# Kernel tuning notes

Hardware: AMD Instinct MI355X
Metric: run time of the kernel (lower is better)

The kernel has to match this reference:

```python
import jax, jax.numpy as jnp
import numpy as np
from jax.scipy.special import gammaln

N, D, RDIM = 2048, 128, 16   # observations, obs dim, simplex dim
R_SAMP = 500                 # importance samples
SIGMA = 0.01
REG = 0.8


def dirichlet_logpdf(x, a):
    # x: [..., r] on simplex, a: broadcastable [..., r] concentrations
    return (jnp.sum((a - 1.0) * jnp.log(x), axis=-1)
            + gammaln(jnp.sum(a, axis=-1))
            - jnp.sum(gammaln(a), axis=-1))


def setup_inputs() -> dict:
    key = jax.random.key(0)
    k1, k2, k3, k4 = jax.random.split(key, 4)
    H = jax.random.uniform(k1, (D, RDIM), dtype=jnp.float32)          # endmember matrix, positive
    alpha = jax.random.uniform(k2, (RDIM,), dtype=jnp.float32) * 2.0 + 0.1
    # realistic observations: y = H z + noise with z ~ Dirichlet(alpha)
    z = jax.random.dirichlet(k3, alpha, shape=(N,)).astype(jnp.float32)  # [N, r]
    y = z @ H.T + jnp.sqrt(SIGMA) * jax.random.normal(k4, (N, D), dtype=jnp.float32)
    return {"y": y, "H": H, "alpha": alpha}


def reference(y, H, alpha):
    sigma = SIGMA
    alpha0 = alpha.sum()
    m = alpha / alpha0                                                  # [r]
    C = (jnp.diag(m) - jnp.outer(m, m)) / (alpha0 + 1.0)                # [r, r]
    EY = H @ m                                                          # [d]
    Cyy = H @ C @ H.T + sigma * jnp.eye(H.shape[0], dtype=jnp.float32)  # [d, d]
    invCyy = jnp.linalg.inv(Cyy)
    gain = C @ H.T @ invCyy                                             # [r, d]
    # LMMSE posterior mean per observation, projected back to simplex
    LMMSE_m = jax.nn.relu(m + (y - EY) @ gain.T) + 1e-6                 # [N, r]
    LMMSE_m = LMMSE_m / LMMSE_m.sum(axis=1, keepdims=True)
    LMMSE_C = C - gain @ H @ C                                          # [r, r]
    trace_C = jax.nn.relu(jnp.trace(LMMSE_C)) + 1e-6
    k = (1.0 - jnp.sum(LMMSE_m ** 2, axis=-1)) / trace_C - 1.0          # [N]
    diri = jax.nn.relu(k[:, None] * LMMSE_m) + REG                      # [N, r]
    # importance sampling: Dirichlet proposal (reparameterized in jax)
    samp = jax.random.dirichlet(jax.random.key(42), diri,
                                shape=(R_SAMP, y.shape[0])).astype(jnp.float32)  # [R, N, r]
    yzSy = jnp.einsum('dr,hnr->nhd', H, samp) - y[:, None, :]           # [N, R, d]
    pyz = jnp.sum(yzSy * yzSy, axis=-1) / (-2.0 * sigma)                # [N, R]
    qz = dirichlet_logpdf(samp, diri).T                                 # [N, R]
    pz = dirichlet_logpdf(samp, alpha).T                                # [N, R]
    weights = jax.nn.softmax(pyz + pz - qz, axis=-1)                    # [N, R]
    zy = jnp.einsum('hnk,nh->nk', samp, weights)                        # [N, r]
    zzy = jnp.einsum('hnk,hnl,nh->nkl', samp, samp, weights)            # [N, r, r]
    return zy, zzy
```

## Files before the change

kernel.cpp:

```cpp
#include <hip/hip_runtime.h>
#include <cstdint>
#include <cmath>

#pragma clang fp contract(off)

#define N_OBS 2048
#define D_DIM 128
#define R_DIM 16
#define NSAMP 500

#define WS_M     0
#define WS_EY    64
#define WS_GAIN  576
#define WS_SCAL  8768
#define WS_G     8800
#define WS_DIRI  279136
#define WS_QC    410208
#define WS_U     418400

__device__ __forceinline__ float flog(float x)   { return (float)log((double)x); }
__device__ __forceinline__ float flog1p(float x) { return (float)log1p((double)x); }

__device__ __forceinline__ void tf_block(uint32_t k0, uint32_t k1,
                                         uint32_t x0, uint32_t x1,
                                         uint32_t& o0, uint32_t& o1) {
  const uint32_t k2 = k0 ^ k1 ^ 0x1BD11BDAu;
  x0 += k0; x1 += k1;
#define TF_R(r) { x0 += x1; x1 = (x1 << (r)) | (x1 >> (32 - (r))); x1 ^= x0; }
  TF_R(13) TF_R(15) TF_R(26) TF_R(6)
  x0 += k1; x1 += k2 + 1u;
  TF_R(17) TF_R(29) TF_R(16) TF_R(24)
  x0 += k2; x1 += k0 + 2u;
  TF_R(13) TF_R(15) TF_R(26) TF_R(6)
  x0 += k0; x1 += k1 + 3u;
  TF_R(17) TF_R(29) TF_R(16) TF_R(24)
  x0 += k1; x1 += k2 + 4u;
  TF_R(13) TF_R(15) TF_R(26) TF_R(6)
  x0 += k2; x1 += k0 + 5u;
#undef TF_R
  o0 = x0; o1 = x1;
}

__device__ __forceinline__ uint32_t rb32(uint32_t ka, uint32_t kb) {
  uint32_t o0, o1;
  tf_block(ka, kb, 0u, 0u, o0, o1);
  return o0 ^ o1;
}

__device__ __forceinline__ float u01(uint32_t bits) {
  uint32_t fb = (bits >> 9) | 0x3F800000u;
  return __uint_as_float(fb) - 1.0f;
}

__device__ __forceinline__ float erfinv_xla(float x) {
  float w = -flog1p(-(x * x));
  float p;
  if (w < 5.0f) {
    w = w - 2.5f;
    p = 2.81022636e-08f;
    p = 3.43273939e-07f + p * w;
    p = -3.5233877e-06f + p * w;
    p = -4.39150654e-06f + p * w;
    p = 0.00021858087f + p * w;
    p = -0.00125372503f + p * w;
    p = -0.00417768164f + p * w;
    p = 0.246640727f + p * w;
    p = 1.50140941f + p * w;
  } else {
    w = sqrtf(w) - 3.0f;
    p = -0.000200214257f;
    p = 0.000100950558f + p * w;
    p = 0.00134934322f + p * w;
    p = -0.00367342844f + p * w;
    p = 0.00573950773f + p * w;
    p = -0.0076224613f + p * w;
    p = 0.00943887047f + p * w;
    p = 1.00167406f + p * w;
    p = 2.83297682f + p * w;
  }
  return p * x;
}

__device__ __forceinline__ float normal_jax(uint32_t ka, uint32_t kb) {
  float f = u01(rb32(ka, kb));
  float u = f * 2.0f + (-0.99999994f);
  u = fmaxf(-0.99999994f, u);
  return 1.41421356f * erfinv_xla(u);
}

__global__ __launch_bounds__(256) void prep_kernel(const float* __restrict__ H,
                                                   const float* __restrict__ alpha,
                                                   char* __restrict__ ws) {
  float* m    = (float*)(ws + WS_M);
  float* EY   = (float*)(ws + WS_EY);
  float* gain = (float*)(ws + WS_GAIN);
  float* scal = (float*)(ws + WS_SCAL);
  float* Gws  = (float*)(ws + WS_G);

  __shared__ float sH[128 * 16];
  __shared__ float sC[16][16];
  __shared__ float sHC[128 * 16];
  __shared__ float sm[16];
  __shared__ double sHtH[16][16];
  __shared__ double M[16][33];
  __shared__ double dfac[16];
  __shared__ double spiv;
  __shared__ int   spivrow;
  __shared__ float sgain[16 * 128];

  int t = threadIdx.x;
  for (int i = t; i < 2048; i += 256) sH[i] = H[i];
  __syncthreads();

  if (t == 0) {
    float a0 = 0.0f;
    for (int j = 0; j < 16; ++j) a0 += alpha[j];
    float pc = lgammaf(a0);
    for (int j = 0; j < 16; ++j) pc -= lgammaf(alpha[j]);
    scal[2] = a0; scal[1] = pc;
    for (int j = 0; j < 16; ++j) { sm[j] = alpha[j] / a0; m[j] = sm[j]; }
  }
  __syncthreads();
  float a0 = scal[2];

  {
    int i = t >> 4, j = t & 15;
    float v = ((i == j) ? sm[i] : 0.0f) - sm[i] * sm[j];
    sC[i][j] = v / (a0 + 1.0f);
  }
  if (t < 128) {
    float acc = 0.0f;
    for (int j = 0; j < 16; ++j) acc += sH[t * 16 + j] * sm[j];
    EY[t] = acc;
  }
  __syncthreads();

  for (int idx = t; idx < 2048; idx += 256) {
    int dd = idx >> 4, j = idx & 15;
    float acc = 0.0f;
    for (int i = 0; i < 16; ++i) acc += sH[dd * 16 + i] * sC[i][j];
    sHC[idx] = acc;
  }
  {
    int i = t >> 4, j = t & 15;
    double acc = 0.0;
    for (int dd = 0; dd < 128; ++dd)
      acc += (double)sH[dd * 16 + i] * (double)sH[dd * 16 + j];
    sHtH[i][j] = acc;
    Gws[i * 16 + j] = (float)acc;
  }
  __syncthreads();

  {
    int i = t >> 4, j = t & 15;
    double acc = (i == j) ? 0.01 : 0.0;
    for (int k = 0; k < 16; ++k) acc += (double)sC[i][k] * sHtH[k][j];
    M[i][j] = acc;
    M[i][16 + j] = (i == j) ? 1.0 : 0.0;
  }
  __syncthreads();

  for (int p = 0; p < 16; ++p) {
    if (t == 0) {
      int best = p; double bv = fabs(M[p][p]);
      for (int r = p + 1; r < 16; ++r) {
        double v = fabs(M[r][p]);
        if (v > bv) { bv = v; best = r; }
      }
      spivrow = best;
    }
    __syncthreads();
    int pr = spivrow;
    double va = 0.0, vb = 0.0;
    if (t < 32 && pr != p) { va = M[p][t]; vb = M[pr][t]; }
    __syncthreads();
    if (t < 32 && pr != p) { M[p][t] = vb; M[pr][t] = va; }
    __syncthreads();
    if (t == 0) spiv = 1.0 / M[p][p];
    __syncthreads();
    if (t < 32) M[p][t] *= spiv;
    if (t < 16) dfac[t] = M[t][p];
    __syncthreads();
    for (int e = t; e < 512; e += 256) {
      int r = e >> 5, c = e & 31;
      if (r != p) M[r][c] -= dfac[r] * M[p][c];
    }
    __syncthreads();
  }

  for (int idx = t; idx < 2048; idx += 256) {
    int j = idx >> 7, dd = idx & 127;
    double acc = 0.0;
    for (int k = 0; k < 16; ++k) acc += M[j][16 + k] * (double)sHC[dd * 16 + k];
    float g = (float)acc;
    sgain[j * 128 + dd] = g;
    gain[j * 128 + dd] = g;
  }
  __syncthreads();

  if (t == 0) {
    float tr = 0.0f;
    for (int j = 0; j < 16; ++j) {
      float s2 = 0.0f;
      for (int dd = 0; dd < 128; ++dd) s2 += sgain[j * 128 + dd] * sHC[dd * 16 + j];
      tr += sC[j][j] - s2;
    }
    tr = fmaxf(tr, 0.0f) + 1e-6f;
    scal[0] = tr;
  }
}

__global__ __launch_bounds__(256) void diri_kernel(const float* __restrict__ y,
                                                   const float* __restrict__ H,
                                                   char* __restrict__ ws) {
  float* m    = (float*)(ws + WS_M);
  float* EY   = (float*)(ws + WS_EY);
  float* gain = (float*)(ws + WS_GAIN);
  float* scal = (float*)(ws + WS_SCAL);
  float* diri = (float*)(ws + WS_DIRI);
  float* cns  = (float*)(ws + WS_QC);
  float* Uws  = (float*)(ws + WS_U);

  __shared__ float sg[16 * 128];
  __shared__ float sH[128 * 16];
  __shared__ float sEY[128];
  __shared__ float sm[16];
  __shared__ float s_tr, s_pc;

  int t = threadIdx.x;
  for (int i = t; i < 2048; i += 256) { sg[i] = gain[i]; sH[i] = H[i]; }
  if (t < 128) sEY[t] = EY[t];
  if (t < 16) sm[t] = m[t];
  if (t == 0) { s_tr = scal[0]; s_pc = scal[1]; }
  __syncthreads();

  int n = blockIdx.x * 256 + t;
  float tv[16], u[16];
#pragma unroll
  for (int j = 0; j < 16; ++j) { tv[j] = sm[j]; u[j] = 0.0f; }
  float yy = 0.0f;
  const float* yn = y + n * 128;
  for (int dd = 0; dd < 128; ++dd) {
    float yv = yn[dd];
    float dy = yv - sEY[dd];
    yy += yv * yv;
#pragma unroll
    for (int j = 0; j < 16; ++j) {
      tv[j] += dy * sg[j * 128 + dd];
      u[j]  += yv * sH[dd * 16 + j];
    }
  }
  float s = 0.0f;
#pragma unroll
  for (int j = 0; j < 16; ++j) { tv[j] = fmaxf(tv[j], 0.0f) + 1e-6f; s += tv[j]; }
  float ssq = 0.0f;
#pragma unroll
  for (int j = 0; j < 16; ++j) { tv[j] = tv[j] / s; ssq += tv[j] * tv[j]; }
  float k = (1.0f - ssq) / s_tr - 1.0f;
  float dsum = 0.0f, lgs = 0.0f;
  float* dn = diri + n * 16;
#pragma unroll
  for (int j = 0; j < 16; ++j) {
    float dj = fmaxf(k * tv[j], 0.0f) + 0.8f;
    dn[j] = dj; dsum += dj; lgs += lgammaf(dj);
    Uws[n * 16 + j] = u[j];
  }
  float qcn = lgammaf(dsum) - lgs;
  cns[n] = s_pc - qcn - 50.0f * yy;
}

__global__ __launch_bounds__(256) void main_kernel(const float* __restrict__ alpha,
                                                   const char* __restrict__ ws,
                                                   float* __restrict__ out) {
  const float* diri = (const float*)(ws + WS_DIRI);
  const float* cns  = (const float*)(ws + WS_QC);
  const float* Uw   = (const float*)(ws + WS_U);
  const float* Gw   = (const float*)(ws + WS_G);

  __shared__ float slg_all[32][256];
  __shared__ float sz[16][17];
  __shared__ float slw[16], swv[16];
  __shared__ float sM, sS, sFac;

  int t = threadIdx.x;
  int n = blockIdx.x;
  int h_sub = t >> 4, j = t & 15;

  float aj = diri[n * 16 + j];

  {
    bool boost = (aj >= 1.0f);
    float aa = boost ? aj : (aj + 1.0f);
    float d  = aa - 0.33333334f;
    float cc = 0.33333334f / sqrtf(d);
    float inv_a = 1.0f / aj;
    float ld32 = logf(d);
    int numc = (h_sub < 4) ? 32 : 31;
    int c = 0;
    bool need_init = true;
    bool pending = true;
    uint32_t kcx = 0, kcy = 0;
    float log_samples = 0.0f;

    while (__ballot(pending)) {
      if (pending) {
        if (need_init) {
          int h = c * 16 + h_sub;
          uint32_t jf = (((uint32_t)h * 2048u + (uint32_t)n) << 4) | (uint32_t)j;
          uint32_t ka, kb, ska, skb;
          tf_block(0u, 42u, 0u, jf, ka, kb);
          tf_block(ka, kb, 0u, 0u, kcx, kcy);
          tf_block(ka, kb, 0u, 1u, ska, skb);
          float ef = u01(rb32(ska, skb));
          log_samples = log1pf(-ef);
          need_init = false;
        }
        uint32_t xka, xkb, Uka, Ukb;
        tf_block(kcx, kcy, 0u, 1u, xka, xkb);
        tf_block(kcx, kcy, 0u, 2u, Uka, Ukb);
        float x = 0.0f, v = -1.0f;
        for (int in = 0; in < 256; ++in) {
          uint32_t sxa, sxb;
          tf_block(xka, xkb, 0u, 1u, sxa, sxb);
          x = normal_jax(sxa, sxb);
          v = 1.0f + x * cc;
          if (v > 0.0f) break;
          uint32_t nxa, nxb;
          tf_block(xka, xkb, 0u, 0u, nxa, nxb);
          xka = nxa; xkb = nxb;
        }
        float X = x * x;
        float V = (v * v) * v;
        float U = u01(rb32(Uka, Ukb));
        float lv32 = logf(V);
        bool cont = (U >= 1.0f - 0.0331f * (X * X));
        if (cont) {
          float lu32  = logf(U);
          float rhs32 = X * 0.5f + d * ((1.0f - V) + lv32);
          float margin = lu32 - rhs32;
          float thr = 4.8e-7f * fabsf(lu32)
                    + 4.8e-7f * d * fabsf(lv32)
                    + 1.2e-7f * (fabsf(rhs32) + X)
                    + 1e-7f;
          if (fabsf(margin) > thr) {
            cont = (margin >= 0.0f);
          } else {
            cont = (flog(U) >= X * 0.5f + d * ((1.0f - V) + flog(V)));
          }
        }
        if (cont) {
          uint32_t kna, knb;
          tf_block(kcx, kcy, 0u, 0u, kna, knb);
          kcx = kna; kcy = knb;
        } else {
          float log_boost = (boost || log_samples == 0.0f)
                              ? 0.0f : log_samples * inv_a;
          slg_all[c][t] = (ld32 + lv32) + log_boost;
          ++c;
          need_init = true;
          pending = (c < numc);
        }
      }
    }
  }

  float Greg[16];
#pragma unroll
  for (int k = 0; k < 16; ++k) Greg[k] = Gw[j * 16 + k];
  float uj2  = 2.0f * Uw[n * 16 + j];
  float cn   = cns[n];
  float admj = alpha[j] - aj;
  if (t == 0) { sM = -INFINITY; sS = 0.0f; sFac = 1.0f; }
  __syncthreads();

  float acc = 0.0f;
  float zyacc = 0.0f;

  for (int cch = 0; cch < 32; ++cch) {
    int h = cch * 16 + h_sub;
    bool valid = (h < NSAMP);
    float lg = slg_all[cch][t];

    float mx = lg;
    mx = fmaxf(mx, __shfl_xor(mx, 1, 16));
    mx = fmaxf(mx, __shfl_xor(mx, 2, 16));
    mx = fmaxf(mx, __shfl_xor(mx, 4, 16));
    mx = fmaxf(mx, __shfl_xor(mx, 8, 16));
    float ez = expf(lg - mx);
    float se = ez;
    se += __shfl_xor(se, 1, 16);
    se += __shfl_xor(se, 2, 16);
    se += __shfl_xor(se, 4, 16);
    se += __shfl_xor(se, 8, 16);
    float z = valid ? (ez / se) : 0.0f;
    sz[h_sub][j] = z;
    float lz = logf(z);
    float pq = admj * lz;

    float gz = 0.0f;
#pragma unroll
    for (int k = 0; k < 16; ++k) gz = fmaf(Greg[k], sz[h_sub][k], gz);
    float sres = z * (gz - uj2);

    pq   += __shfl_xor(pq, 1, 16);
    pq   += __shfl_xor(pq, 2, 16);
    pq   += __shfl_xor(pq, 4, 16);
    pq   += __shfl_xor(pq, 8, 16);
    sres += __shfl_xor(sres, 1, 16);
    sres += __shfl_xor(sres, 2, 16);
    sres += __shfl_xor(sres, 4, 16);
    sres += __shfl_xor(sres, 8, 16);

    if (j == 0) {
      float lw = -50.0f * sres + pq + cn;
      slw[h_sub] = valid ? lw : -INFINITY;
    }
    __syncthreads();

    if (t < 16) {
      float cmax = sM;
      for (int hh = 0; hh < 16; ++hh) cmax = fmaxf(cmax, slw[hh]);
      float w = expf(slw[t] - cmax);
      swv[t] = w;
      if (t == 0) {
        float f2 = expf(sM - cmax);
        float Snew = sS * f2;
        for (int hh = 0; hh < 16; ++hh) Snew += swv[hh];
        sM = cmax; sS = Snew; sFac = f2;
      }
    }
    __syncthreads();

    float fc = sFac;
    acc *= fc;
#pragma unroll
    for (int hh = 0; hh < 16; ++hh)
      acc = fmaf(swv[hh] * sz[hh][h_sub], sz[hh][j], acc);
    if (t < 16) {
      zyacc *= fc;
#pragma unroll
      for (int hh = 0; hh < 16; ++hh) zyacc = fmaf(swv[hh], sz[hh][t], zyacc);
    }
    __syncthreads();
  }

  float Sf = sS;
  if (t < 16) out[n * 16 + t] = zyacc / Sf;
  out[N_OBS * R_DIM + n * 256 + t] = acc / Sf;
}

extern "C" void kernel_launch(void* const* d_in, const int* in_sizes, int n_in,
                              void* d_out, int out_size, void* d_ws, size_t ws_size,
                              hipStream_t stream) {
  const float* y     = (const float*)d_in[0];
  const float* H     = (const float*)d_in[1];
  const float* alpha = (const float*)d_in[2];
  char* ws = (char*)d_ws;
  float* out = (float*)d_out;

  prep_kernel<<<1, 256, 0, stream>>>(H, alpha, ws);
  diri_kernel<<<8, 256, 0, stream>>>(y, H, ws);
  main_kernel<<<N_OBS, 256, 0, stream>>>(alpha, ws, out);
}
```

Before: 629.3 us.

## Use float32 erfinv log with error-bounded fallback; fold diri kernel into main

The gamma rejection sampler now computes the erfinv log term with float32 log1pf instead of the double-precision version. It tracks an error bound and recomputes exactly with doubles only when a branch decision (v sign, squeeze test, log test) falls within that bound. The separate diri kernel is removed and its per-observation LMMSE/Dirichlet-parameter work is recomputed inside main_kernel per block, reusing the sample shared buffer. The prep kernel also shrinks to 64 threads. The goal is to avoid costly double log1p in the hot inner loop and a kernel launch, at the cost of extra per-block setup work and more complex bit-exactness logic.

```diff
diff --git a/kernel.cpp b/kernel.cpp
--- a/kernel.cpp
+++ b/kernel.cpp
@@ -14,9 +14,6 @@
 #define WS_GAIN  576
 #define WS_SCAL  8768
 #define WS_G     8800
-#define WS_DIRI  279136
-#define WS_QC    410208
-#define WS_U     418400
 
 __device__ __forceinline__ float flog(float x)   { return (float)log((double)x); }
 __device__ __forceinline__ float flog1p(float x) { return (float)log1p((double)x); }
@@ -52,11 +49,10 @@
   return __uint_as_float(fb) - 1.0f;
 }
 
-__device__ __forceinline__ float erfinv_xla(float x) {
-  float w = -flog1p(-(x * x));
+__device__ __forceinline__ float erfinv_poly(float w0) {
   float p;
-  if (w < 5.0f) {
-    w = w - 2.5f;
+  if (w0 < 5.0f) {
+    float w = w0 - 2.5f;
     p = 2.81022636e-08f;
     p = 3.43273939e-07f + p * w;
     p = -3.5233877e-06f + p * w;
@@ -67,7 +63,7 @@
     p = 0.246640727f + p * w;
     p = 1.50140941f + p * w;
   } else {
-    w = sqrtf(w) - 3.0f;
+    float w = sqrtf(w0) - 3.0f;
     p = -0.000200214257f;
     p = 0.000100950558f + p * w;
     p = 0.00134934322f + p * w;
@@ -78,19 +74,17 @@
     p = 1.00167406f + p * w;
     p = 2.83297682f + p * w;
   }
-  return p * x;
-}
-
-__device__ __forceinline__ float normal_jax(uint32_t ka, uint32_t kb) {
-  float f = u01(rb32(ka, kb));
-  float u = f * 2.0f + (-0.99999994f);
-  u = fmaxf(-0.99999994f, u);
-  return 1.41421356f * erfinv_xla(u);
-}
-
-__global__ __launch_bounds__(256) void prep_kernel(const float* __restrict__ H,
-                                                   const float* __restrict__ alpha,
-                                                   char* __restrict__ ws) {
+  return p;
+}
+
+__device__ __forceinline__ float normal_exact_from_u(float uu) {
+  float w = -flog1p(-(uu * uu));
+  return 1.41421356f * (erfinv_poly(w) * uu);
+}
+
+__global__ __launch_bounds__(64) void prep_kernel(const float* __restrict__ H,
+                                                  const float* __restrict__ alpha,
+                                                  char* __restrict__ ws) {
   float* m    = (float*)(ws + WS_M);
   float* EY   = (float*)(ws + WS_EY);
   float* gain = (float*)(ws + WS_GAIN);
@@ -109,7 +103,7 @@
   __shared__ float sgain[16 * 128];
 
   int t = threadIdx.x;
-  for (int i = t; i < 2048; i += 256) sH[i] = H[i];
+  for (int i = t; i < 2048; i += 64) sH[i] = H[i];
   __syncthreads();
 
   if (t == 0) {
@@ -123,26 +117,26 @@
   __syncthreads();
   float a0 = scal[2];
 
-  {
-    int i = t >> 4, j = t & 15;
+  for (int e = t; e < 256; e += 64) {
+    int i = e >> 4, j = e & 15;
     float v = ((i == j) ? sm[i] : 0.0f) - sm[i] * sm[j];
     sC[i][j] = v / (a0 + 1.0f);
   }
-  if (t < 128) {
+  for (int dd = t; dd < 128; dd += 64) {
     float acc = 0.0f;
-    for (int j = 0; j < 16; ++j) acc += sH[t * 16 + j] * sm[j];
-    EY[t] = acc;
-  }
-  __syncthreads();
-
-  for (int idx = t; idx < 2048; idx += 256) {
+    for (int j = 0; j < 16; ++j) acc += sH[dd * 16 + j] * sm[j];
+    EY[dd] = acc;
+  }
+  __syncthreads();
+
+  for (int idx = t; idx < 2048; idx += 64) {
     int dd = idx >> 4, j = idx & 15;
     float acc = 0.0f;
     for (int i = 0; i < 16; ++i) acc += sH[dd * 16 + i] * sC[i][j];
     sHC[idx] = acc;
   }
-  {
-    int i = t >> 4, j = t & 15;
+  for (int e = t; e < 256; e += 64) {
+    int i = e >> 4, j = e & 15;
     double acc = 0.0;
     for (int dd = 0; dd < 128; ++dd)
       acc += (double)sH[dd * 16 + i] * (double)sH[dd * 16 + j];
@@ -151,8 +145,8 @@
   }
   __syncthreads();
 
-  {
-    int i = t >> 4, j = t & 15;
+  for (int e = t; e < 256; e += 64) {
+    int i = e >> 4, j = e & 15;
     double acc = (i == j) ? 0.01 : 0.0;
     for (int k = 0; k < 16; ++k) acc += (double)sC[i][k] * sHtH[k][j];
     M[i][j] = acc;
@@ -181,14 +175,14 @@
     if (t < 32) M[p][t] *= spiv;
     if (t < 16) dfac[t] = M[t][p];
     __syncthreads();
-    for (int e = t; e < 512; e += 256) {
+    for (int e = t; e < 512; e += 64) {
       int r = e >> 5, c = e & 31;
       if (r != p) M[r][c] -= dfac[r] * M[p][c];
     }
     __syncthreads();
   }
 
-  for (int idx = t; idx < 2048; idx += 256) {
+  for (int idx = t; idx < 2048; idx += 64) {
     int j = idx >> 7, dd = idx & 127;
     double acc = 0.0;
     for (int k = 0; k < 16; ++k) acc += M[j][16 + k] * (double)sHC[dd * 16 + k];
@@ -210,83 +204,79 @@
   }
 }
 
-__global__ __launch_bounds__(256) void diri_kernel(const float* __restrict__ y,
-                                                   const float* __restrict__ H,
-                                                   char* __restrict__ ws) {
-  float* m    = (float*)(ws + WS_M);
-  float* EY   = (float*)(ws + WS_EY);
-  float* gain = (float*)(ws + WS_GAIN);
-  float* scal = (float*)(ws + WS_SCAL);
-  float* diri = (float*)(ws + WS_DIRI);
-  float* cns  = (float*)(ws + WS_QC);
-  float* Uws  = (float*)(ws + WS_U);
-
-  __shared__ float sg[16 * 128];
-  __shared__ float sH[128 * 16];
-  __shared__ float sEY[128];
-  __shared__ float sm[16];
-  __shared__ float s_tr, s_pc;
-
-  int t = threadIdx.x;
-  for (int i = t; i < 2048; i += 256) { sg[i] = gain[i]; sH[i] = H[i]; }
-  if (t < 128) sEY[t] = EY[t];
-  if (t < 16) sm[t] = m[t];
-  if (t == 0) { s_tr = scal[0]; s_pc = scal[1]; }
-  __syncthreads();
-
-  int n = blockIdx.x * 256 + t;
-  float tv[16], u[16];
-#pragma unroll
-  for (int j = 0; j < 16; ++j) { tv[j] = sm[j]; u[j] = 0.0f; }
-  float yy = 0.0f;
-  const float* yn = y + n * 128;
-  for (int dd = 0; dd < 128; ++dd) {
-    float yv = yn[dd];
-    float dy = yv - sEY[dd];
-    yy += yv * yv;
-#pragma unroll
-    for (int j = 0; j < 16; ++j) {
-      tv[j] += dy * sg[j * 128 + dd];
-      u[j]  += yv * sH[dd * 16 + j];
-    }
-  }
-  float s = 0.0f;
-#pragma unroll
-  for (int j = 0; j < 16; ++j) { tv[j] = fmaxf(tv[j], 0.0f) + 1e-6f; s += tv[j]; }
-  float ssq = 0.0f;
-#pragma unroll
-  for (int j = 0; j < 16; ++j) { tv[j] = tv[j] / s; ssq += tv[j] * tv[j]; }
-  float k = (1.0f - ssq) / s_tr - 1.0f;
-  float dsum = 0.0f, lgs = 0.0f;
-  float* dn = diri + n * 16;
-#pragma unroll
-  for (int j = 0; j < 16; ++j) {
-    float dj = fmaxf(k * tv[j], 0.0f) + 0.8f;
-    dn[j] = dj; dsum += dj; lgs += lgammaf(dj);
-    Uws[n * 16 + j] = u[j];
-  }
-  float qcn = lgammaf(dsum) - lgs;
-  cns[n] = s_pc - qcn - 50.0f * yy;
-}
-
-__global__ __launch_bounds__(256) void main_kernel(const float* __restrict__ alpha,
+__global__ __launch_bounds__(256) void main_kernel(const float* __restrict__ y,
+                                                   const float* __restrict__ Hg,
+                                                   const float* __restrict__ alpha,
                                                    const char* __restrict__ ws,
                                                    float* __restrict__ out) {
-  const float* diri = (const float*)(ws + WS_DIRI);
-  const float* cns  = (const float*)(ws + WS_QC);
-  const float* Uw   = (const float*)(ws + WS_U);
+  const float* mws  = (const float*)(ws + WS_M);
+  const float* EYw  = (const float*)(ws + WS_EY);
+  const float* gain = (const float*)(ws + WS_GAIN);
+  const float* scal = (const float*)(ws + WS_SCAL);
   const float* Gw   = (const float*)(ws + WS_G);
 
   __shared__ float slg_all[32][256];
   __shared__ float sz[16][17];
   __shared__ float slw[16], swv[16];
+  __shared__ float sdiri[16], su2[16], stv[16];
+  __shared__ float smisc[2];
   __shared__ float sM, sS, sFac;
 
   int t = threadIdx.x;
   int n = blockIdx.x;
   int h_sub = t >> 4, j = t & 15;
 
-  float aj = diri[n * 16 + j];
+  {
+    float* sGainT = &slg_all[0][0];
+    float* sHs    = sGainT + 2048;
+    float* sys    = sHs + 2048;
+    float* sEYs   = sys + 128;
+    for (int i = t; i < 2048; i += 256) {
+      sGainT[(i & 127) * 16 + (i >> 7)] = gain[i];
+      sHs[i] = Hg[i];
+    }
+    if (t < 128) { sys[t] = y[n * 128 + t]; sEYs[t] = EYw[t]; }
+    __syncthreads();
+    if (t < 16) {
+      float tv = mws[t];
+      float u = 0.0f;
+      for (int dd = 0; dd < 128; ++dd) {
+        float yv = sys[dd];
+        float dy = yv - sEYs[dd];
+        tv += dy * sGainT[dd * 16 + t];
+        u  += yv * sHs[dd * 16 + t];
+      }
+      stv[t] = tv;
+      su2[t] = 2.0f * u;
+    }
+    __syncthreads();
+    if (t == 0) {
+      float yy = 0.0f;
+      for (int dd = 0; dd < 128; ++dd) yy += sys[dd] * sys[dd];
+      float s = 0.0f;
+      for (int jj = 0; jj < 16; ++jj) {
+        float v = fmaxf(stv[jj], 0.0f) + 1e-6f; stv[jj] = v; s += v;
+      }
+      float ssq = 0.0f;
+      for (int jj = 0; jj < 16; ++jj) {
+        float v = stv[jj] / s; stv[jj] = v; ssq += v * v;
+      }
+      float k = (1.0f - ssq) / scal[0] - 1.0f;
+      float dsum = 0.0f, lgs = 0.0f;
+      for (int jj = 0; jj < 16; ++jj) {
+        float dj = fmaxf(k * stv[jj], 0.0f) + 0.8f;
+        sdiri[jj] = dj; dsum += dj; lgs += lgammaf(dj);
+      }
+      float qcn = lgammaf(dsum) - lgs;
+      smisc[0] = scal[1] - qcn - 50.0f * yy;
+    }
+    __syncthreads();
+  }
+
+  float aj   = sdiri[j];
+  float uj2  = su2[j];
+  float cn   = smisc[0];
+  float admj = alpha[j] - aj;
 
   {
     bool boost = (aj >= 1.0f);
@@ -318,12 +308,25 @@
         uint32_t xka, xkb, Uka, Ukb;
         tf_block(kcx, kcy, 0u, 1u, xka, xkb);
         tf_block(kcx, kcy, 0u, 2u, Uka, Ukb);
-        float x = 0.0f, v = -1.0f;
+        float x = 0.0f, v = -1.0f, ex = 0.0f, uu = 0.0f;
         for (int in = 0; in < 256; ++in) {
           uint32_t sxa, sxb;
           tf_block(xka, xkb, 0u, 1u, sxa, sxb);
-          x = normal_jax(sxa, sxb);
+          float f = u01(rb32(sxa, sxb));
+          uu = fmaxf(-0.99999994f, f * 2.0f + (-0.99999994f));
+          float w32 = -log1pf(-(uu * uu));
+          if (fabsf(w32 - 5.0f) < 4e-6f) {
+            x = normal_exact_from_u(uu); ex = 0.0f;
+          } else {
+            x = 1.41421356f * (erfinv_poly(w32) * uu);
+            ex = (w32 < 5.0f) ? (5e-7f * fabsf(uu) * w32 + 1e-9f)
+                              : (1e-6f * fabsf(uu) * sqrtf(w32) + 1e-9f);
+          }
           v = 1.0f + x * cc;
+          if (fabsf(v) <= 2.0f * cc * ex + 1e-9f) {
+            x = normal_exact_from_u(uu); ex = 0.0f;
+            v = 1.0f + x * cc;
+          }
           if (v > 0.0f) break;
           uint32_t nxa, nxb;
           tf_block(xka, xkb, 0u, 0u, nxa, nxb);
@@ -333,20 +336,35 @@
         float V = (v * v) * v;
         float U = u01(rb32(Uka, Ukb));
         float lv32 = logf(V);
-        bool cont = (U >= 1.0f - 0.0331f * (X * X));
-        if (cont) {
+        bool cont = false;
+        bool need_exact = false;
+        float sqz = 1.0f - 0.0331f * (X * X);
+        float ms  = U - sqz;
+        float thr_s = 0.3f * fabsf(x) * X * ex + 1e-10f;
+        if (fabsf(ms) <= thr_s) {
+          need_exact = true;
+        } else if (ms < 0.0f) {
+          cont = false;
+        } else {
           float lu32  = logf(U);
           float rhs32 = X * 0.5f + d * ((1.0f - V) + lv32);
           float margin = lu32 - rhs32;
           float thr = 4.8e-7f * fabsf(lu32)
                     + 4.8e-7f * d * fabsf(lv32)
                     + 1.2e-7f * (fabsf(rhs32) + X)
-                    + 1e-7f;
-          if (fabsf(margin) > thr) {
-            cont = (margin >= 0.0f);
-          } else {
-            cont = (flog(U) >= X * 0.5f + d * ((1.0f - V) + flog(V)));
+                    + 1e-7f
+                    + ex * (2.0f * fabsf(x) + 8.0f * d * cc * fabsf(1.0f - V) / v);
+          if (fabsf(margin) > thr) cont = (margin >= 0.0f);
+          else need_exact = true;
+        }
+        if (need_exact) {
+          if (ex > 0.0f) {
+            x = normal_exact_from_u(uu);
+            v = 1.0f + x * cc; X = x * x; V = (v * v) * v;
+            lv32 = logf(V);
           }
+          cont = (U >= 1.0f - 0.0331f * (X * X));
+          if (cont) cont = (flog(U) >= X * 0.5f + d * ((1.0f - V) + flog(V)));
         }
         if (cont) {
           uint32_t kna, knb;
@@ -367,9 +385,6 @@
   float Greg[16];
 #pragma unroll
   for (int k = 0; k < 16; ++k) Greg[k] = Gw[j * 16 + k];
-  float uj2  = 2.0f * Uw[n * 16 + j];
-  float cn   = cns[n];
-  float admj = alpha[j] - aj;
   if (t == 0) { sM = -INFINITY; sS = 0.0f; sFac = 1.0f; }
   __syncthreads();
 
@@ -458,7 +473,6 @@
   char* ws = (char*)d_ws;
   float* out = (float*)d_out;
 
-  prep_kernel<<<1, 256, 0, stream>>>(H, alpha, ws);
-  diri_kernel<<<8, 256, 0, stream>>>(y, H, ws);
-  main_kernel<<<N_OBS, 256, 0, stream>>>(alpha, ws, out);
-}
+  prep_kernel<<<1, 64, 0, stream>>>(H, alpha, ws);
+  main_kernel<<<N_OBS, 256, 0, stream>>>(y, H, alpha, ws, out);
+}
```

New measurement: 657.4 us. 1.04x slower.
